# Kernel optimization log

Hardware: AMD Instinct MI355X
Metric: run time of the kernel (lower is better)

The kernel has to match this reference:

```python
import jax, jax.numpy as jnp
import numpy as np

D_MODEL = 1024
N_EXPERTS = 8
TOP_K = 2
CAP_FACTOR = 1.0
HIDDEN = 2816  # multiple_of*ceil(int(2*4*d/3)/multiple_of) with multiple_of=256


def setup_inputs() -> dict:
    key = jax.random.key(0)
    ks = jax.random.split(key, 8)
    B, S = 2, 2048
    s = 0.02
    return {
        "x": jax.random.normal(ks[0], (B, S, D_MODEL), jnp.float32),
        "noise": jax.random.normal(ks[1], (B, S, N_EXPERTS), jnp.float32),
        "router_w": jax.random.normal(ks[2], (N_EXPERTS, D_MODEL), jnp.float32) * s,
        "router_b": jnp.zeros((N_EXPERTS,), jnp.float32),
        "noise_w": jax.random.normal(ks[3], (N_EXPERTS, D_MODEL), jnp.float32) * s,
        "noise_b": jnp.zeros((N_EXPERTS,), jnp.float32),
        "w1": jax.random.normal(ks[4], (N_EXPERTS, HIDDEN, D_MODEL), jnp.float32) * s,
        "w3": jax.random.normal(ks[5], (N_EXPERTS, HIDDEN, D_MODEL), jnp.float32) * s,
        "w2": jax.random.normal(ks[6], (N_EXPERTS, D_MODEL, HIDDEN), jnp.float32) * s,
    }


def reference(x, noise, router_w, router_b, noise_w, noise_b, w1, w3, w2):
    B, S, d = x.shape
    N = B * S
    capacity = int(N * TOP_K / N_EXPERTS * CAP_FACTOR)
    flat_x = x.reshape(N, d)

    # noisy top-k router
    logits = flat_x @ router_w.T + router_b                      # [N, E]
    noise_logits = flat_x @ noise_w.T + noise_b                  # [N, E]
    noisy = logits + noise.reshape(N, N_EXPERTS) * jax.nn.softplus(noise_logits)
    topv, topi = jax.lax.top_k(noisy, TOP_K)                     # [N, k]
    # softmax over sparse (-inf filled) logits == softmax over top-k values
    gw = jax.nn.softmax(topv, axis=-1)                           # [N, k]

    updates = jnp.zeros_like(flat_x)
    tok_ids = jnp.arange(N, dtype=jnp.int32)
    for e in range(N_EXPERTS):
        hit = topi == e                                          # [N, k]
        gate = jnp.sum(gw * hit, axis=-1)                        # [N]
        m = jnp.any(hit, axis=-1)                                # token routed to e
        pos = jnp.cumsum(m.astype(jnp.int32)) - 1                # rank in flat order
        keep = m & (pos < capacity)                              # capacity truncation (first-come)
        slot = jnp.where(keep, pos, capacity)                    # dropped tokens -> overflow slot
        # gather tokens into fixed-capacity buffer (slot `capacity` is a trash slot)
        buf = jnp.zeros((capacity + 1, d), x.dtype).at[slot].set(flat_x)
        tok = jnp.full((capacity + 1,), N, jnp.int32).at[slot].set(tok_ids)
        xb = buf[:capacity]
        # SwiGLU FFN: w2( silu(x w1^T) * (x w3^T) )
        h = jax.nn.silu(xb @ w1[e].T) * (xb @ w3[e].T)           # [cap, H]
        o = h @ w2[e].T                                          # [cap, d]
        tke = tok[:capacity]
        g = jnp.where(tke < N, gate[jnp.clip(tke, 0, N - 1)], 0.0)
        # scatter-combine; index N drops (empty slots)
        updates = updates.at[tke].add(o * g[:, None], mode="drop")
    return updates.reshape(B, S, d)
```

## Files before the change

kernel.cpp:

```cpp
#include <hip/hip_runtime.h>


#define D_MODEL 1024
#define HIDDEN 2816
#define N_TOK 4096
#define CAP 1024

typedef __attribute__((ext_vector_type(8))) short short8;
typedef __attribute__((ext_vector_type(4))) float f32x4;

__device__ __forceinline__ unsigned short f2bf(float f) {
  unsigned int u = __float_as_uint(f);
  u += 0x7fffu + ((u >> 16) & 1u);
  return (unsigned short)(u >> 16);
}
__device__ __forceinline__ float bf2f(unsigned short h) {
  return __uint_as_float(((unsigned int)h) << 16);
}

template <int Ncnt> __device__ __forceinline__ void waitv() {
  if constexpr (Ncnt == 8)      asm volatile("s_waitcnt vmcnt(8)" ::: "memory");
  else if constexpr (Ncnt == 6) asm volatile("s_waitcnt vmcnt(6)" ::: "memory");
  else                          asm volatile("s_waitcnt vmcnt(0)" ::: "memory");
}

__global__ void router_kernel(const float* __restrict__ x, const float* __restrict__ noise,
                              const float* __restrict__ rw, const float* __restrict__ rb,
                              const float* __restrict__ nw, const float* __restrict__ nb,
                              int* __restrict__ topi, float* __restrict__ gall,
                              int* __restrict__ slot) {
  int wid = threadIdx.x >> 6;
  int lane = threadIdx.x & 63;
  int t = blockIdx.x * 4 + wid;
  if (t >= N_TOK) return;
  const float* xr = x + (size_t)t * D_MODEL;
  double accL[8] = {0,0,0,0,0,0,0,0};
  double accN[8] = {0,0,0,0,0,0,0,0};
  for (int i = 0; i < 4; ++i) {
    int kb = (i * 64 + lane) * 4;
    float4 xv = *(const float4*)(xr + kb);
#pragma unroll
    for (int e = 0; e < 8; ++e) {
      float4 wv = *(const float4*)(rw + e * D_MODEL + kb);
      accL[e] += (double)xv.x * wv.x + (double)xv.y * wv.y + (double)xv.z * wv.z + (double)xv.w * wv.w;
      float4 nv = *(const float4*)(nw + e * D_MODEL + kb);
      accN[e] += (double)xv.x * nv.x + (double)xv.y * nv.y + (double)xv.z * nv.z + (double)xv.w * nv.w;
    }
  }
#pragma unroll
  for (int e = 0; e < 8; ++e) {
    for (int s = 32; s > 0; s >>= 1) {
      accL[e] += __shfl_xor(accL[e], s);
      accN[e] += __shfl_xor(accN[e], s);
    }
  }
  if (lane == 0) {
    double noisy[8];
#pragma unroll
    for (int e = 0; e < 8; ++e) {
      double lg = accL[e] + (double)rb[e];
      double nl = accN[e] + (double)nb[e];
      double sp = (nl > 0.0 ? nl : 0.0) + log1p(exp(-fabs(nl)));
      noisy[e] = lg + (double)noise[t * 8 + e] * sp;
    }
    int i0 = 0;
    for (int e = 1; e < 8; ++e) if (noisy[e] > noisy[i0]) i0 = e;
    int i1 = -1;
    for (int e = 0; e < 8; ++e) { if (e == i0) continue; if (i1 < 0 || noisy[e] > noisy[i1]) i1 = e; }
    double g0 = 1.0 / (1.0 + exp(noisy[i1] - noisy[i0]));
    topi[t * 2] = i0; topi[t * 2 + 1] = i1;
    gall[t * 2] = (float)g0; gall[t * 2 + 1] = (float)(1.0 - g0);
    slot[t * 2] = -1; slot[t * 2 + 1] = -1;
  }
}

__global__ void scan_kernel(const int* __restrict__ topi,
                            int* __restrict__ slot, int* __restrict__ tok_list) {
  int e = blockIdx.x;
  int tid = threadIdx.x;
  int lane = tid & 63, wid = tid >> 6;
  __shared__ int wsum[16];
  __shared__ int base_s;
  tok_list[e * CAP + tid] = -1;
  if (tid == 0) base_s = 0;
  __syncthreads();
  for (int chunk = 0; chunk < N_TOK / 1024; ++chunk) {
    int t = chunk * 1024 + tid;
    int i0 = topi[t * 2], i1 = topi[t * 2 + 1];
    bool m = (i0 == e) || (i1 == e);
    unsigned long long mask = __ballot(m);
    int excl = __popcll(mask & ((1ull << lane) - 1ull));
    if (lane == 0) wsum[wid] = __popcll(mask);
    __syncthreads();
    int base = base_s;
    int woff = 0;
    for (int w = 0; w < wid; ++w) woff += wsum[w];
    int pos = base + woff + excl;
    if (m && pos < CAP) {
      tok_list[e * CAP + pos] = t;
      if (i0 == e) slot[t * 2] = pos; else slot[t * 2 + 1] = pos;
    }
    __syncthreads();
    if (tid == 0) {
      int s = 0;
      for (int w = 0; w < 16; ++w) s += wsum[w];
      base_s = base + s;
    }
    __syncthreads();
  }
}

__global__ void gather_kernel(const float* __restrict__ x, const int* __restrict__ tok_list,
                              unsigned short* __restrict__ xb) {
  int row = blockIdx.x;
  int tok = tok_list[row];
  unsigned short* dst = xb + (size_t)row * D_MODEL + threadIdx.x * 4;
  if (tok < 0) {
    *(ushort4*)dst = make_ushort4(0, 0, 0, 0);
  } else {
    float4 v = *(const float4*)(x + (size_t)tok * D_MODEL + threadIdx.x * 4);
    *(ushort4*)dst = make_ushort4(f2bf(v.x), f2bf(v.y), f2bf(v.z), f2bf(v.w));
  }
}

__global__ void cvt3_kernel(const float* __restrict__ s0, const float* __restrict__ s1,
                            const float* __restrict__ s2, unsigned short* __restrict__ d0,
                            unsigned short* __restrict__ d1, unsigned short* __restrict__ d2) {
  int i = blockIdx.x * blockDim.x + threadIdx.x;
  const float* src = (blockIdx.y == 0) ? s0 : (blockIdx.y == 1) ? s1 : s2;
  unsigned short* dst = (blockIdx.y == 0) ? d0 : (blockIdx.y == 1) ? d1 : d2;
  float4 v = *(const float4*)(src + (size_t)i * 4);
  *(ushort4*)(dst + (size_t)i * 4) = make_ushort4(f2bf(v.x), f2bf(v.y), f2bf(v.z), f2bf(v.w));
}

template <int NOUT, int K, int NW, int MODE>
__global__ __launch_bounds__(512, 1)
void gemm_moe(const unsigned short* __restrict__ Ab, const unsigned short* __restrict__ B0,
              const unsigned short* __restrict__ B1, void* __restrict__ OUT) {
  constexpr int ABYTES = 32768;
  constexpr int BUFSZ = ABYTES + NW * 16384;
  constexpr int KT = K / 64;
  constexpr int SK = (MODE == 2) ? 2 : 1;
  constexpr int KTS = KT / SK;
  constexpr int BNCOL = (MODE == 2 && NW == 2) ? 256 : 128;
  constexpr int NBN = NOUT / BNCOL;
  constexpr int NWG = 8 * 4 * NBN * SK;
  constexpr int CPW = (32 + NW * 16) / 8;

  __shared__ char smem[2 * BUFSZ];

  int lid = blockIdx.x;
  int swz = (lid & 7) * (NWG / 8) + (lid >> 3);
  constexpr int PERE = 4 * NBN * SK;
  int e = swz / PERE;
  int r = swz - e * PERE;
  int bm = r / (NBN * SK);
  int r2 = r - bm * (NBN * SK);
  int bn = r2 / SK;
  int sk = r2 - bn * SK;
  int kt0 = sk * KTS;

  const unsigned short* A = Ab + (size_t)e * CAP * K;
  int tid = threadIdx.x, lane = tid & 63, wid = tid >> 6;
  int wr = wid >> 2, wc = wid & 3;
  int lane15 = lane & 15, lhi = lane >> 4, l7 = lane & 7;

  int lrow = lane >> 3;
  int lcol = ((lane & 7) ^ lrow) * 8;
  const unsigned short* Abase = A + (size_t)(bm * 256 + lrow) * K + lcol;
  const unsigned short* Bb0 = B0 + (size_t)e * NOUT * K + (size_t)(bn * BNCOL + lrow) * K + lcol;
  const unsigned short* Bb1 = (NW == 2)
      ? B1 + (size_t)e * NOUT * K + (size_t)(bn * BNCOL + lrow) * K + lcol : Bb0;

  auto STAGE = [&](int ktile, int buf) {
    char* lb = smem + buf * BUFSZ;
#pragma unroll
    for (int i = 0; i < CPW; ++i) {
      int c = wid * CPW + i;
      if (c < 32) {
        const unsigned short* g = Abase + (size_t)(c * 8) * K + ktile * 64;
        __builtin_amdgcn_global_load_lds((const __attribute__((address_space(1))) void*)g,
                                         (__attribute__((address_space(3))) void*)(lb + c * 1024), 16, 0, 0);
      } else {
        int cb2 = c - 32;
        const unsigned short* base = (cb2 >> 4) ? Bb1 : Bb0;
        const unsigned short* g = base + (size_t)((cb2 & 15) * 8) * K + ktile * 64;
        __builtin_amdgcn_global_load_lds((const __attribute__((address_space(1))) void*)g,
                                         (__attribute__((address_space(3))) void*)(lb + ABYTES + cb2 * 1024), 16, 0, 0);
      }
    }
  };

  int sw0 = ((0 + lhi) ^ l7) * 16;
  int sw1 = ((4 + lhi) ^ l7) * 16;

  f32x4 acc[8][NW][2] = {};

  STAGE(kt0, 0);
  STAGE(kt0 + 1, 1);
  waitv<CPW>();
  __builtin_amdgcn_sched_barrier(0);
  __builtin_amdgcn_s_barrier();
  __builtin_amdgcn_sched_barrier(0);

  for (int ktl = 0; ktl < KTS; ++ktl) {
    char* cb = smem + (ktl & 1) * BUFSZ;
    short8 a0[8], b0[NW][2], a1[8], b1[NW][2];
#pragma unroll
    for (int w = 0; w < NW; ++w)
#pragma unroll
      for (int n = 0; n < 2; ++n)
        b0[w][n] = *(const short8*)(cb + ABYTES + w * 16384 + wc * 4096 + n * 2048 + lane15 * 128 + sw0);
#pragma unroll
    for (int m = 0; m < 8; ++m)
      a0[m] = *(const short8*)(cb + wr * 16384 + m * 2048 + lane15 * 128 + sw0);
    __builtin_amdgcn_s_setprio(1);
#pragma unroll
    for (int m = 0; m < 8; ++m)
#pragma unroll
      for (int w = 0; w < NW; ++w)
#pragma unroll
        for (int n = 0; n < 2; ++n)
          acc[m][w][n] = __builtin_amdgcn_mfma_f32_16x16x32_bf16(a0[m], b0[w][n], acc[m][w][n], 0, 0, 0);
    __builtin_amdgcn_s_setprio(0);
#pragma unroll
    for (int w = 0; w < NW; ++w)
#pragma unroll
      for (int n = 0; n < 2; ++n)
        b1[w][n] = *(const short8*)(cb + ABYTES + w * 16384 + wc * 4096 + n * 2048 + lane15 * 128 + sw1);
#pragma unroll
    for (int m = 0; m < 8; ++m)
      a1[m] = *(const short8*)(cb + wr * 16384 + m * 2048 + lane15 * 128 + sw1);
    __builtin_amdgcn_sched_barrier(0);
    __builtin_amdgcn_s_barrier();
    __builtin_amdgcn_sched_barrier(0);
    if (ktl + 2 < KTS) STAGE(kt0 + ktl + 2, ktl & 1);
    __builtin_amdgcn_s_setprio(1);
#pragma unroll
    for (int m = 0; m < 8; ++m)
#pragma unroll
      for (int w = 0; w < NW; ++w)
#pragma unroll
        for (int n = 0; n < 2; ++n)
          acc[m][w][n] = __builtin_amdgcn_mfma_f32_16x16x32_bf16(a1[m], b1[w][n], acc[m][w][n], 0, 0, 0);
    __builtin_amdgcn_s_setprio(0);
    if (ktl + 2 < KTS) waitv<CPW>();
    else if (ktl + 1 < KTS) waitv<0>();
    __builtin_amdgcn_sched_barrier(0);
    if (ktl + 1 < KTS) __builtin_amdgcn_s_barrier();
    __builtin_amdgcn_sched_barrier(0);
  }

  if constexpr (MODE == 1) {
    unsigned short* H = (unsigned short*)OUT + (size_t)e * CAP * NOUT;
#pragma unroll
    for (int m = 0; m < 8; ++m) {
#pragma unroll
      for (int n = 0; n < 2; ++n) {
        int row0 = bm * 256 + wr * 128 + m * 16 + lhi * 4;
        int col = bn * 128 + wc * 32 + n * 16 + lane15;
#pragma unroll
        for (int j = 0; j < 4; ++j) {
          float g1 = acc[m][0][n][j];
          float g3 = acc[m][1][n][j];
          float hv = g1 / (1.0f + __expf(-g1)) * g3;
          H[(size_t)(row0 + j) * NOUT + col] = f2bf(hv);
        }
      }
    }
  } else {
    float* P = (float*)OUT + (size_t)sk * 8 * CAP * NOUT + (size_t)e * CAP * NOUT;
#pragma unroll
    for (int m = 0; m < 8; ++m) {
#pragma unroll
      for (int w = 0; w < NW; ++w) {
#pragma unroll
        for (int n = 0; n < 2; ++n) {
          int row0 = bm * 256 + wr * 128 + m * 16 + lhi * 4;
          int col = bn * BNCOL + w * 128 + wc * 32 + n * 16 + lane15;
#pragma unroll
          for (int j = 0; j < 4; ++j)
            P[(size_t)(row0 + j) * NOUT + col] = acc[m][w][n][j];
        }
      }
    }
  }
}

__global__ void combine_kernel(const float* __restrict__ ob, const int* __restrict__ topi,
                               const float* __restrict__ gall, const int* __restrict__ slot,
                               float* __restrict__ out) {
  int t = blockIdx.x;
  int d = threadIdx.x * 4;
  const size_t HALF = (size_t)8 * CAP * D_MODEL;
  float4 r = make_float4(0.f, 0.f, 0.f, 0.f);
#pragma unroll
  for (int k = 0; k < 2; ++k) {
    int s = slot[t * 2 + k];
    if (s >= 0) {
      int e = topi[t * 2 + k];
      float g = gall[t * 2 + k];
      size_t base = ((size_t)e * CAP + s) * D_MODEL + d;
      float4 a = *(const float4*)(ob + base);
      float4 b = *(const float4*)(ob + HALF + base);
      r.x += g * (a.x + b.x); r.y += g * (a.y + b.y);
      r.z += g * (a.z + b.z); r.w += g * (a.w + b.w);
    }
  }
  *(float4*)(out + (size_t)t * D_MODEL + d) = r;
}

extern "C" void kernel_launch(void* const* d_in, const int* in_sizes, int n_in,
                              void* d_out, int out_size, void* d_ws, size_t ws_size,
                              hipStream_t stream) {
  const float* x     = (const float*)d_in[0];
  const float* noise = (const float*)d_in[1];
  const float* rw    = (const float*)d_in[2];
  const float* rb    = (const float*)d_in[3];
  const float* nw    = (const float*)d_in[4];
  const float* nb    = (const float*)d_in[5];
  const float* w1    = (const float*)d_in[6];
  const float* w3    = (const float*)d_in[7];
  const float* w2    = (const float*)d_in[8];
  float* out = (float*)d_out;

  char* ws = (char*)d_ws;
  size_t off = 0;
  auto alloc = [&](size_t bytes) -> void* {
    void* p = ws + off;
    off += (bytes + 255) & ~(size_t)255;
    return p;
  };
  const size_t WELEM = (size_t)8 * HIDDEN * D_MODEL;
  unsigned short* wb1 = (unsigned short*)alloc(WELEM * 2);
  unsigned short* wb3 = (unsigned short*)alloc(WELEM * 2);
  unsigned short* wb2 = (unsigned short*)alloc(WELEM * 2);
  unsigned short* xb  = (unsigned short*)alloc((size_t)8 * CAP * D_MODEL * 2);
  unsigned short* h   = (unsigned short*)alloc((size_t)8 * CAP * HIDDEN * 2);
  float*          ob  = (float*)alloc((size_t)2 * 8 * CAP * D_MODEL * 4);
  int*   topi  = (int*)alloc(N_TOK * 2 * 4);
  float* gall  = (float*)alloc(N_TOK * 2 * 4);
  int*   slot  = (int*)alloc(N_TOK * 2 * 4);
  int*   tokl  = (int*)alloc(8 * CAP * 4);
  (void)ws_size; (void)in_sizes; (void)n_in; (void)out_size;

  const int n4w = (int)(WELEM / 4);
  cvt3_kernel<<<dim3(n4w / 256, 3), 256, 0, stream>>>(w1, w3, w2, wb1, wb3, wb2);

  router_kernel<<<N_TOK / 4, 256, 0, stream>>>(x, noise, rw, rb, nw, nb, topi, gall, slot);
  scan_kernel<<<8, 1024, 0, stream>>>(topi, slot, tokl);
  gather_kernel<<<8 * CAP, 256, 0, stream>>>(x, tokl, xb);

  gemm_moe<HIDDEN, D_MODEL, 2, 1><<<dim3(704), 512, 0, stream>>>(xb, wb1, wb3, (void*)h);

  gemm_moe<D_MODEL, HIDDEN, 2, 2><<<dim3(256), 512, 0, stream>>>(
      h, wb2, wb2 + (size_t)128 * HIDDEN, (void*)ob);

  combine_kernel<<<N_TOK, 256, 0, stream>>>(ob, topi, gall, slot, out);
}
```

Before: 323.4 us.

## Fuse fp32-to-bf16 weight conversion into MoE GEMM loaders

Removes the separate pass that converted all expert weights to bf16. The GEMM kernels now load fp32 weight tiles into registers, pack them to bf16 with a hardware convert instruction, and write them to LDS. A pipeline stage and new wait counts are added. This avoids a full extra read and write of the weight tensors, but each workgroup reads twice the bytes per weight tile and does the conversion in-loop.

```diff
diff --git a/kernel.cpp b/kernel.cpp
--- a/kernel.cpp
+++ b/kernel.cpp
@@ -17,10 +17,15 @@
 __device__ __forceinline__ float bf2f(unsigned short h) {
   return __uint_as_float(((unsigned int)h) << 16);
 }
+__device__ __forceinline__ unsigned cvtpk(float lo, float hi) {
+  unsigned r;
+  asm("v_cvt_pk_bf16_f32 %0, %1, %2" : "=v"(r) : "v"(lo), "v"(hi));
+  return r;
+}
 
 template <int Ncnt> __device__ __forceinline__ void waitv() {
-  if constexpr (Ncnt == 8)      asm volatile("s_waitcnt vmcnt(8)" ::: "memory");
-  else if constexpr (Ncnt == 6) asm volatile("s_waitcnt vmcnt(6)" ::: "memory");
+  if constexpr (Ncnt == 12)     asm volatile("s_waitcnt vmcnt(12)" ::: "memory");
+  else if constexpr (Ncnt == 4) asm volatile("s_waitcnt vmcnt(4)" ::: "memory");
   else                          asm volatile("s_waitcnt vmcnt(0)" ::: "memory");
 }
 
@@ -123,29 +128,18 @@
   }
 }
 
-__global__ void cvt3_kernel(const float* __restrict__ s0, const float* __restrict__ s1,
-                            const float* __restrict__ s2, unsigned short* __restrict__ d0,
-                            unsigned short* __restrict__ d1, unsigned short* __restrict__ d2) {
-  int i = blockIdx.x * blockDim.x + threadIdx.x;
-  const float* src = (blockIdx.y == 0) ? s0 : (blockIdx.y == 1) ? s1 : s2;
-  unsigned short* dst = (blockIdx.y == 0) ? d0 : (blockIdx.y == 1) ? d1 : d2;
-  float4 v = *(const float4*)(src + (size_t)i * 4);
-  *(ushort4*)(dst + (size_t)i * 4) = make_ushort4(f2bf(v.x), f2bf(v.y), f2bf(v.z), f2bf(v.w));
-}
-
-template <int NOUT, int K, int NW, int MODE>
+template <int NOUT, int K, int MODE>
 __global__ __launch_bounds__(512, 1)
-void gemm_moe(const unsigned short* __restrict__ Ab, const unsigned short* __restrict__ B0,
-              const unsigned short* __restrict__ B1, void* __restrict__ OUT) {
+void gemm_moe(const unsigned short* __restrict__ Ab, const float* __restrict__ W0,
+              const float* __restrict__ W1, void* __restrict__ OUT) {
   constexpr int ABYTES = 32768;
-  constexpr int BUFSZ = ABYTES + NW * 16384;
+  constexpr int BUFSZ = ABYTES + 32768;
   constexpr int KT = K / 64;
   constexpr int SK = (MODE == 2) ? 2 : 1;
   constexpr int KTS = KT / SK;
-  constexpr int BNCOL = (MODE == 2 && NW == 2) ? 256 : 128;
+  constexpr int BNCOL = (MODE == 2) ? 256 : 128;
   constexpr int NBN = NOUT / BNCOL;
   constexpr int NWG = 8 * 4 * NBN * SK;
-  constexpr int CPW = (32 + NW * 16) / 8;
 
   __shared__ char smem[2 * BUFSZ];
 
@@ -168,46 +162,85 @@
   int lrow = lane >> 3;
   int lcol = ((lane & 7) ^ lrow) * 8;
   const unsigned short* Abase = A + (size_t)(bm * 256 + lrow) * K + lcol;
-  const unsigned short* Bb0 = B0 + (size_t)e * NOUT * K + (size_t)(bn * BNCOL + lrow) * K + lcol;
-  const unsigned short* Bb1 = (NW == 2)
-      ? B1 + (size_t)e * NOUT * K + (size_t)(bn * BNCOL + lrow) * K + lcol : Bb0;
-
-  auto STAGE = [&](int ktile, int buf) {
+
+  auto ASTAGE = [&](int ktile, int buf) {
     char* lb = smem + buf * BUFSZ;
 #pragma unroll
-    for (int i = 0; i < CPW; ++i) {
-      int c = wid * CPW + i;
-      if (c < 32) {
-        const unsigned short* g = Abase + (size_t)(c * 8) * K + ktile * 64;
-        __builtin_amdgcn_global_load_lds((const __attribute__((address_space(1))) void*)g,
-                                         (__attribute__((address_space(3))) void*)(lb + c * 1024), 16, 0, 0);
-      } else {
-        int cb2 = c - 32;
-        const unsigned short* base = (cb2 >> 4) ? Bb1 : Bb0;
-        const unsigned short* g = base + (size_t)((cb2 & 15) * 8) * K + ktile * 64;
-        __builtin_amdgcn_global_load_lds((const __attribute__((address_space(1))) void*)g,
-                                         (__attribute__((address_space(3))) void*)(lb + ABYTES + cb2 * 1024), 16, 0, 0);
-      }
+    for (int i = 0; i < 4; ++i) {
+      int c = wid * 4 + i;
+      const unsigned short* g = Abase + (size_t)(c * 8) * K + ktile * 64;
+      __builtin_amdgcn_global_load_lds((const __attribute__((address_space(1))) void*)g,
+                                       (__attribute__((address_space(3))) void*)(lb + c * 1024), 16, 0, 0);
+    }
+  };
+
+  const float* wptr[4];
+  int woff[4];
+#pragma unroll
+  for (int i = 0; i < 4; ++i) {
+    int L = i * 512 + tid;
+    int p = (L >> 3) & 127;
+    int ks = L & 7;
+    const float* Wb = (i >> 1) ? W1 : W0;
+    wptr[i] = Wb + (size_t)e * NOUT * K + (size_t)(bn * BNCOL + p) * K + ks * 8;
+    woff[i] = ABYTES + (i >> 1) * 16384 + p * 128 + ((ks ^ (p & 7)) * 16);
+  }
+
+  float4 rbuf[4][2];
+  auto BLOAD = [&](int ktile) {
+#pragma unroll
+    for (int i = 0; i < 4; ++i) {
+      const float* s = wptr[i] + (size_t)ktile * 64;
+      rbuf[i][0] = *(const float4*)(s);
+      rbuf[i][1] = *(const float4*)(s + 4);
+    }
+  };
+  auto BWRITE = [&](char* lb) {
+#pragma unroll
+    for (int i = 0; i < 4; ++i) {
+      uint4 v;
+      v.x = cvtpk(rbuf[i][0].x, rbuf[i][0].y);
+      v.y = cvtpk(rbuf[i][0].z, rbuf[i][0].w);
+      v.z = cvtpk(rbuf[i][1].x, rbuf[i][1].y);
+      v.w = cvtpk(rbuf[i][1].z, rbuf[i][1].w);
+      *(uint4*)(lb + woff[i]) = v;
     }
   };
 
   int sw0 = ((0 + lhi) ^ l7) * 16;
   int sw1 = ((4 + lhi) ^ l7) * 16;
 
-  f32x4 acc[8][NW][2] = {};
-
-  STAGE(kt0, 0);
-  STAGE(kt0 + 1, 1);
-  waitv<CPW>();
+  f32x4 acc[8][2][2] = {};
+
+  BLOAD(kt0);
+  __builtin_amdgcn_sched_barrier(0);
+  ASTAGE(kt0, 0);
+  __builtin_amdgcn_sched_barrier(0);
+  waitv<4>();
+  BWRITE(smem);
+  BLOAD(kt0 + 1);
+  __builtin_amdgcn_sched_barrier(0);
+  ASTAGE(kt0 + 1, 1);
+  waitv<12>();
+  asm volatile("s_waitcnt lgkmcnt(0)" ::: "memory");
   __builtin_amdgcn_sched_barrier(0);
   __builtin_amdgcn_s_barrier();
   __builtin_amdgcn_sched_barrier(0);
 
   for (int ktl = 0; ktl < KTS; ++ktl) {
     char* cb = smem + (ktl & 1) * BUFSZ;
-    short8 a0[8], b0[NW][2], a1[8], b1[NW][2];
-#pragma unroll
-    for (int w = 0; w < NW; ++w)
+    char* nbuf = smem + ((ktl + 1) & 1) * BUFSZ;
+    if (ktl + 1 < KTS) {
+      waitv<4>();
+      BWRITE(nbuf);
+      if (ktl + 2 < KTS) {
+        BLOAD(kt0 + ktl + 2);
+        __builtin_amdgcn_sched_barrier(0);
+      }
+    }
+    short8 a0[8], b0[2][2], a1[8], b1[2][2];
+#pragma unroll
+    for (int w = 0; w < 2; ++w)
 #pragma unroll
       for (int n = 0; n < 2; ++n)
         b0[w][n] = *(const short8*)(cb + ABYTES + w * 16384 + wc * 4096 + n * 2048 + lane15 * 128 + sw0);
@@ -218,13 +251,13 @@
 #pragma unroll
     for (int m = 0; m < 8; ++m)
 #pragma unroll
-      for (int w = 0; w < NW; ++w)
+      for (int w = 0; w < 2; ++w)
 #pragma unroll
         for (int n = 0; n < 2; ++n)
           acc[m][w][n] = __builtin_amdgcn_mfma_f32_16x16x32_bf16(a0[m], b0[w][n], acc[m][w][n], 0, 0, 0);
     __builtin_amdgcn_s_setprio(0);
 #pragma unroll
-    for (int w = 0; w < NW; ++w)
+    for (int w = 0; w < 2; ++w)
 #pragma unroll
       for (int n = 0; n < 2; ++n)
         b1[w][n] = *(const short8*)(cb + ABYTES + w * 16384 + wc * 4096 + n * 2048 + lane15 * 128 + sw1);
@@ -234,21 +267,24 @@
     __builtin_amdgcn_sched_barrier(0);
     __builtin_amdgcn_s_barrier();
     __builtin_amdgcn_sched_barrier(0);
-    if (ktl + 2 < KTS) STAGE(kt0 + ktl + 2, ktl & 1);
+    if (ktl + 2 < KTS) ASTAGE(kt0 + ktl + 2, ktl & 1);
     __builtin_amdgcn_s_setprio(1);
 #pragma unroll
     for (int m = 0; m < 8; ++m)
 #pragma unroll
-      for (int w = 0; w < NW; ++w)
+      for (int w = 0; w < 2; ++w)
 #pragma unroll
         for (int n = 0; n < 2; ++n)
           acc[m][w][n] = __builtin_amdgcn_mfma_f32_16x16x32_bf16(a1[m], b1[w][n], acc[m][w][n], 0, 0, 0);
     __builtin_amdgcn_s_setprio(0);
-    if (ktl + 2 < KTS) waitv<CPW>();
-    else if (ktl + 1 < KTS) waitv<0>();
-    __builtin_amdgcn_sched_barrier(0);
-    if (ktl + 1 < KTS) __builtin_amdgcn_s_barrier();
-    __builtin_amdgcn_sched_barrier(0);
+    if (ktl + 1 < KTS) {
+      if (ktl + 2 < KTS) waitv<12>();
+      else               waitv<0>();
+      asm volatile("s_waitcnt lgkmcnt(0)" ::: "memory");
+      __builtin_amdgcn_sched_barrier(0);
+      __builtin_amdgcn_s_barrier();
+      __builtin_amdgcn_sched_barrier(0);
+    }
   }
 
   if constexpr (MODE == 1) {
@@ -273,7 +309,7 @@
 #pragma unroll
     for (int m = 0; m < 8; ++m) {
 #pragma unroll
-      for (int w = 0; w < NW; ++w) {
+      for (int w = 0; w < 2; ++w) {
 #pragma unroll
         for (int n = 0; n < 2; ++n) {
           int row0 = bm * 256 + wr * 128 + m * 16 + lhi * 4;
@@ -331,30 +367,23 @@
     off += (bytes + 255) & ~(size_t)255;
     return p;
   };
-  const size_t WELEM = (size_t)8 * HIDDEN * D_MODEL;
-  unsigned short* wb1 = (unsigned short*)alloc(WELEM * 2);
-  unsigned short* wb3 = (unsigned short*)alloc(WELEM * 2);
-  unsigned short* wb2 = (unsigned short*)alloc(WELEM * 2);
-  unsigned short* xb  = (unsigned short*)alloc((size_t)8 * CAP * D_MODEL * 2);
-  unsigned short* h   = (unsigned short*)alloc((size_t)8 * CAP * HIDDEN * 2);
-  float*          ob  = (float*)alloc((size_t)2 * 8 * CAP * D_MODEL * 4);
+  unsigned short* xb = (unsigned short*)alloc((size_t)8 * CAP * D_MODEL * 2);
+  unsigned short* h  = (unsigned short*)alloc((size_t)8 * CAP * HIDDEN * 2);
+  float*          ob = (float*)alloc((size_t)2 * 8 * CAP * D_MODEL * 4);
   int*   topi  = (int*)alloc(N_TOK * 2 * 4);
   float* gall  = (float*)alloc(N_TOK * 2 * 4);
   int*   slot  = (int*)alloc(N_TOK * 2 * 4);
   int*   tokl  = (int*)alloc(8 * CAP * 4);
   (void)ws_size; (void)in_sizes; (void)n_in; (void)out_size;
 
-  const int n4w = (int)(WELEM / 4);
-  cvt3_kernel<<<dim3(n4w / 256, 3), 256, 0, stream>>>(w1, w3, w2, wb1, wb3, wb2);
-
   router_kernel<<<N_TOK / 4, 256, 0, stream>>>(x, noise, rw, rb, nw, nb, topi, gall, slot);
   scan_kernel<<<8, 1024, 0, stream>>>(topi, slot, tokl);
   gather_kernel<<<8 * CAP, 256, 0, stream>>>(x, tokl, xb);
 
-  gemm_moe<HIDDEN, D_MODEL, 2, 1><<<dim3(704), 512, 0, stream>>>(xb, wb1, wb3, (void*)h);
-
-  gemm_moe<D_MODEL, HIDDEN, 2, 2><<<dim3(256), 512, 0, stream>>>(
-      h, wb2, wb2 + (size_t)128 * HIDDEN, (void*)ob);
+  gemm_moe<HIDDEN, D_MODEL, 1><<<dim3(704), 512, 0, stream>>>(xb, w1, w3, (void*)h);
+
+  gemm_moe<D_MODEL, HIDDEN, 2><<<dim3(256), 512, 0, stream>>>(
+      h, w2, w2 + (size_t)128 * HIDDEN, (void*)ob);
 
   combine_kernel<<<N_TOK, 256, 0, stream>>>(ob, topi, gall, slot, out);
 }
```

After: 308.1 us. 1.05x faster.
